# Optimization experiments

Hardware: AMD Instinct MI355X
Metric: run time of the kernel (lower is better)

Reference implementation:

```python
import jax, jax.numpy as jnp
import numpy as np

B, T = 16, 2048
D_MODEL, D_INNER, D_STATE, D_CONV, DT_RANK = 64, 128, 16, 4, 4

def leaky(x):
    return jnp.where(x >= 0, x, 0.01 * x)

def silu(x):
    return x * jax.nn.sigmoid(x)

def conv1d(x, w, b, pad):
    # x: (b,c,t), w: (o,i,k)
    y = jax.lax.conv_general_dilated(x, w, (1,), [(pad, pad)],
        dimension_numbers=('NCH', 'OIH', 'NCH'))
    return y + b[None, :, None]

def pixel_shuffle_1d(x, r):
    b, cr, t = x.shape
    c = cr // r
    return x.reshape(b, c, r, t).transpose(0, 1, 3, 2).reshape(b, c, t * r)

def rmsnorm(x, w, eps=1e-5):
    return x * jax.lax.rsqrt(jnp.mean(x * x, -1, keepdims=True) + eps) * w

def batchnorm(x, g, b, eps=1e-5):
    # training-mode BatchNorm1d: stats over (N, T) per channel
    mu = jnp.mean(x, axis=(0, 2), keepdims=True)
    var = jnp.var(x, axis=(0, 2), keepdims=True)
    return (x - mu) * jax.lax.rsqrt(var + eps) * g[None, :, None] + b[None, :, None]

def selective_scan(u, delta, A, Bm, Cm, D):
    # u, delta: (b,t,d); Bm, Cm: (b,t,n); A: (d,n); D: (d,)
    def step(h, inp):
        d_t, u_t, B_t, C_t = inp  # (b,d),(b,d),(b,n),(b,n)
        dA = jnp.exp(d_t[:, :, None] * A[None])              # (b,d,n)
        h = h * dA + (d_t * u_t)[:, :, None] * B_t[:, None, :]
        y = jnp.einsum('bdn,bn->bd', h, C_t)
        return h, y
    h0 = jnp.zeros((u.shape[0], A.shape[0], A.shape[1]), u.dtype)
    xs = tuple(jnp.swapaxes(a, 0, 1) for a in (delta, u, Bm, Cm))
    _, ys = jax.lax.scan(step, h0, xs)
    return jnp.swapaxes(ys, 0, 1) + u * D[None, None, :]

def mamba_layer(x, norm_w, in_proj_w, dwconv_w, dwconv_b, x_proj_w,
                dt_proj_w, dt_proj_b, A_log, D, out_proj_w):
    # x: (b,t,d_model); pre-norm residual Mamba block
    xn = rmsnorm(x, norm_w)
    xz = xn @ in_proj_w.T                                    # (b,t,2*d_inner)
    xm, z = jnp.split(xz, 2, axis=-1)
    # causal depthwise conv over time (pad left d_conv-1)
    xc = jax.lax.conv_general_dilated(jnp.swapaxes(xm, 1, 2), dwconv_w,
        (1,), [(D_CONV - 1, 0)], dimension_numbers=('NCH', 'OIH', 'NCH'),
        feature_group_count=D_INNER) + dwconv_b[None, :, None]
    xm = silu(jnp.swapaxes(xc, 1, 2))                        # (b,t,d_inner)
    x_dbl = xm @ x_proj_w.T                                  # (b,t,dt_rank+2n)
    dt, Bm, Cm = jnp.split(x_dbl, [DT_RANK, DT_RANK + D_STATE], axis=-1)
    delta = jax.nn.softplus(dt @ dt_proj_w.T + dt_proj_b)    # (b,t,d_inner)
    A = -jnp.exp(A_log)                                      # (d_inner,n)
    y = selective_scan(xm, delta, A, Bm, Cm, D)
    y = y * silu(z)
    return x + y @ out_proj_w.T

def setup_inputs():
    key = jax.random.key(0)
    ks = jax.random.split(key, 16)
    p = lambda k, shp, s=0.02: jax.random.normal(k, shp, jnp.float32) * s
    return {
        'x': jax.random.normal(ks[0], (B, 12, T), jnp.float32),
        'conv_in_w': p(ks[1], (D_MODEL, 12, 15)), 'conv_in_b': jnp.zeros((D_MODEL,), jnp.float32),
        'norm_w': jnp.ones((D_MODEL,), jnp.float32),
        'in_proj_w': p(ks[2], (2 * D_INNER, D_MODEL)),
        'dwconv_w': p(ks[3], (D_INNER, 1, D_CONV), 0.2), 'dwconv_b': jnp.zeros((D_INNER,), jnp.float32),
        'x_proj_w': p(ks[4], (DT_RANK + 2 * D_STATE, D_INNER)),
        'dt_proj_w': p(ks[5], (D_INNER, DT_RANK), 0.5),
        'dt_proj_b': jnp.full((D_INNER,), -2.0, jnp.float32),
        'A_log': jnp.tile(jnp.log(jnp.arange(1, D_STATE + 1, dtype=jnp.float32))[None], (D_INNER, 1)),
        'D': jnp.ones((D_INNER,), jnp.float32),
        'out_proj_w': p(ks[6], (D_MODEL, D_INNER)),
        'merge_w': p(ks[7], (D_MODEL, D_MODEL, 15)), 'merge_b': jnp.zeros((D_MODEL,), jnp.float32),
        'bn_g': jnp.ones((D_MODEL,), jnp.float32), 'bn_b': jnp.zeros((D_MODEL,), jnp.float32),
        'up1_w': p(ks[8], (320 * 5, D_MODEL, 15)), 'up1_b': jnp.zeros((320 * 5,), jnp.float32),
        'up2_w': p(ks[9], (128 * 2, 320, 15)), 'up2_b': jnp.zeros((128 * 2,), jnp.float32),
        'out_w': p(ks[10], (12, 128, 15)), 'out_b': jnp.zeros((12,), jnp.float32),
    }

def reference(x, conv_in_w, conv_in_b, norm_w, in_proj_w, dwconv_w, dwconv_b,
              x_proj_w, dt_proj_w, dt_proj_b, A_log, D, out_proj_w,
              merge_w, merge_b, bn_g, bn_b, up1_w, up1_b, up2_w, up2_b,
              out_w, out_b):
    h = leaky(conv1d(x, conv_in_w, conv_in_b, 7))            # (b,64,t)
    hold = h
    s = mamba_layer(jnp.swapaxes(h, 1, 2), norm_w, in_proj_w, dwconv_w,
                    dwconv_b, x_proj_w, dt_proj_w, dt_proj_b, A_log, D,
                    out_proj_w)
    h2 = jnp.swapaxes(s, 1, 2)                               # (b,64,t)
    m = batchnorm(conv1d(h2, merge_w, merge_b, 7), bn_g, bn_b) + hold
    u5 = leaky(pixel_shuffle_1d(conv1d(m, up1_w, up1_b, 7), 5))    # (b,320,5t)
    u10 = leaky(pixel_shuffle_1d(conv1d(u5, up2_w, up2_b, 7), 2))  # (b,128,10t)
    return conv1d(u10, out_w, out_b, 7)                      # (b,12,10t)
```

## Files before the change

kernel.cpp:

```cpp
#include <hip/hip_runtime.h>
#include <hip/hip_bf16.h>
#include <math.h>

typedef __hip_bfloat16 bf16;
typedef __attribute__((ext_vector_type(8))) short short8;
typedef __attribute__((ext_vector_type(4))) float f32x4;

#define BB 16
#define TT 2048
#define DM 64
#define DI 128
#define DSN 16
#define NCHK 32
#define CLEN 64

union U8 { int4 i4; unsigned short u[8]; };

__device__ __forceinline__ bf16  f2b(float v){ return __float2bfloat16(v); }
__device__ __forceinline__ float b2f(bf16 v){ return __bfloat162float(v); }
__device__ __forceinline__ unsigned short f2bu(float v){
  bf16 b = __float2bfloat16(v); unsigned short u; __builtin_memcpy(&u,&b,2); return u;
}
__device__ __forceinline__ float bu2f(unsigned short u){
  unsigned int x = ((unsigned int)u) << 16; float f; __builtin_memcpy(&f,&x,4); return f;
}
__device__ __forceinline__ float siluf(float x){ return x / (1.f + __expf(-x)); }
__device__ __forceinline__ float leakyf(float x){ return x >= 0.f ? x : 0.01f*x; }
__device__ __forceinline__ float softplusf(float x){ return x > 20.f ? x : log1pf(__expf(x)); }

struct PackCfg { const float* w; short* wp; int COUT, CIN, NTg, NCH, NTAP, fragOff; };
struct PackArgs { PackCfg c[7]; int totalFrags; float* stats; };

__global__ __launch_bounds__(256) void k_pack_all(PackArgs a)
{
  int i = blockIdx.x*256 + threadIdx.x;
  if (blockIdx.x == 0 && threadIdx.x < 128) a.stats[threadIdx.x] = 0.f;
  int lane = i & 63, frag = i >> 6;
  if (frag >= a.totalFrags) return;
  int ci_ = 0;
  #pragma unroll
  for (int q = 1; q < 7; q++) if (frag >= a.c[q].fragOff) ci_ = q;
  const PackCfg& C = a.c[ci_];
  int lf = frag - C.fragOff;
  int cot = lf % C.NTg; int kc = lf / C.NTg;
  int ch = kc % C.NCH;  int k  = kc / C.NCH;
  int co = cot*16 + (lane & 15);
  int ci0 = ch*32 + (lane >> 4)*8;
  unsigned short v[8];
  #pragma unroll
  for (int j = 0; j < 8; j++)
    v[j] = (co < C.COUT) ? f2bu(C.w[((size_t)co*C.CIN + ci0 + j)*C.NTAP + k]) : (unsigned short)0;
  short* dst = C.wp + (size_t)lf*512 + lane*8;
  *(int4*)dst = *(int4*)v;
}

__global__ __launch_bounds__(256) void k_conv_in(
    const float* __restrict__ x, const float* __restrict__ w,
    const float* __restrict__ bias, bf16* __restrict__ ht)
{
  __shared__ float sx[12][272];
  __shared__ float sw[12][15];
  int tid = threadIdx.x;
  int t0 = blockIdx.x * 256;
  int co = blockIdx.y;
  int b  = blockIdx.z;
  for (int i = tid; i < 12*15; i += 256) sw[i/15][i%15] = w[co*180 + i];
  for (int i = tid; i < 12*270; i += 256) {
    int ci = i/270, L = i%270;
    int tt = t0 - 7 + L;
    sx[ci][L] = (tt >= 0 && tt < TT) ? x[((size_t)b*12+ci)*TT + tt] : 0.f;
  }
  __syncthreads();
  float acc = bias[co];
  #pragma unroll
  for (int ci = 0; ci < 12; ci++) {
    #pragma unroll
    for (int k = 0; k < 15; k++)
      acc += sx[ci][tid+k]*sw[ci][k];
  }
  acc = leakyf(acc);
  int t = t0 + tid;
  ht[((size_t)b*TT + t)*DM + co] = f2b(acc);
}

__global__ __launch_bounds__(256) void k_inproj_mfma(
    const bf16* __restrict__ ht, const float* __restrict__ nw,
    const short* __restrict__ wp, bf16* __restrict__ xm, bf16* __restrict__ z)
{
  __shared__ short sxa[64*128];
  __shared__ float sred[64][4];
  const int tid = threadIdx.x;
  const int lane = tid & 63, wv = tid >> 6;
  const int lnm = lane & 15, quad = lane >> 4;
  const size_t bt0 = (size_t)blockIdx.x * 64;

  {
    int row = tid >> 2, part = tid & 3, ch0 = part*16;
    const short* src = (const short*)ht + (bt0 + row)*64 + ch0;
    U8 p0, p1; p0.i4 = *(const int4*)src; p1.i4 = *(const int4*)(src + 8);
    float f[16]; float ss = 0.f;
    #pragma unroll
    for (int j = 0; j < 8; j++) { f[j] = bu2f(p0.u[j]); f[8+j] = bu2f(p1.u[j]); }
    #pragma unroll
    for (int j = 0; j < 16; j++) ss += f[j]*f[j];
    sred[row][part] = ss;
    __syncthreads();
    float tot = sred[row][0]+sred[row][1]+sred[row][2]+sred[row][3];
    float sc = rsqrtf(tot*(1.f/64.f) + 1e-5f);
    U8 o0, o1;
    #pragma unroll
    for (int j = 0; j < 8; j++) {
      o0.u[j] = f2bu(f[j]  *sc*nw[ch0+j]);
      o1.u[j] = f2bu(f[8+j]*sc*nw[ch0+8+j]);
    }
    int s0 = part*2, s1 = part*2+1;
    *(int4*)(sxa + row*128 + ((s0 ^ (row&7))<<3)) = o0.i4;
    *(int4*)(sxa + row*128 + ((s1 ^ (row&7))<<3)) = o1.i4;
  }
  __syncthreads();

  f32x4 acc[4][4];
  #pragma unroll
  for (int m = 0; m < 4; m++)
    #pragma unroll
    for (int n = 0; n < 4; n++) acc[m][n] = (f32x4){0.f,0.f,0.f,0.f};

  #pragma unroll
  for (int kc = 0; kc < 2; kc++) {
    short8 bfr[4];
    #pragma unroll
    for (int n = 0; n < 4; n++) {
      int fid = kc*16 + wv*4 + n;
      bfr[n] = *(const short8*)(wp + (size_t)fid*512 + lane*8);
    }
    #pragma unroll
    for (int m = 0; m < 4; m++) {
      int r2 = m*16 + lnm;
      short8 a = *(const short8*)(sxa + r2*128 + (((kc*4+quad) ^ (r2&7))<<3));
      #pragma unroll
      for (int n = 0; n < 4; n++)
        acc[m][n] = __builtin_amdgcn_mfma_f32_16x16x32_bf16(a, bfr[n], acc[m][n], 0, 0, 0);
    }
  }

  #pragma unroll
  for (int m = 0; m < 4; m++)
    #pragma unroll
    for (int n = 0; n < 4; n++) {
      int co = wv*64 + n*16 + lnm;
      float v[4] = {acc[m][n].x, acc[m][n].y, acc[m][n].z, acc[m][n].w};
      #pragma unroll
      for (int r = 0; r < 4; r++) {
        size_t t = bt0 + m*16 + quad*4 + r;
        if (co < 128) xm[t*128 + co]       = f2b(v[r]);
        else          z [t*128 + (co-128)] = f2b(v[r]);
      }
    }
}

__global__ __launch_bounds__(256) void k_dwconv(
    const bf16* __restrict__ xm, const float* __restrict__ w,
    const float* __restrict__ bias, bf16* __restrict__ xcb)
{
  int idx = blockIdx.x*256 + threadIdx.x;
  int c = idx & (DI-1);
  int bt = idx >> 7;
  int t = bt & (TT-1);
  float acc = bias[c];
  #pragma unroll
  for (int k = 0; k < 4; k++) {
    int tt = t - 3 + k;
    if (tt >= 0) acc += b2f(xm[(size_t)(bt - 3 + k)*DI + c]) * w[c*4+k];
  }
  xcb[idx] = f2b(siluf(acc));
}

__global__ __launch_bounds__(256) void k_xproj_mfma(
    const bf16* __restrict__ xcb, const short* __restrict__ wp, float* __restrict__ xd)
{
  __shared__ __align__(16) char smem[256*64];
  const int tid = threadIdx.x;
  const int lane = tid & 63, wv = tid >> 6;
  const int lnm = lane & 15, quad = lane >> 4;
  const size_t bt0 = (size_t)blockIdx.x * 256;
  const int wvt = wv*64;

  f32x4 acc[4][3];
  #pragma unroll
  for (int m = 0; m < 4; m++)
    #pragma unroll
    for (int n = 0; n < 3; n++) acc[m][n] = (f32x4){0.f,0.f,0.f,0.f};

  for (int ch = 0; ch < 4; ch++) {
    __syncthreads();
    int sl = tid & 3;
    for (int r = tid >> 2; r < 256; r += 64) {
      int4 v = *(const int4*)((const short*)xcb + (bt0 + r)*128 + ch*32 + sl*8);
      *(int4*)(&smem[r*64 + ((sl ^ ((r>>1) & 3)) << 4)]) = v;
    }
    __syncthreads();
    short8 bfr[3];
    #pragma unroll
    for (int n = 0; n < 3; n++)
      bfr[n] = *(const short8*)(wp + (size_t)(ch*3+n)*512 + lane*8);
    #pragma unroll
    for (int m = 0; m < 4; m++) {
      int row = wvt + m*16 + lnm;
      short8 a = *(const short8*)(&smem[row*64 + ((quad ^ ((row>>1) & 3)) << 4)]);
      #pragma unroll
      for (int n = 0; n < 3; n++)
        acc[m][n] = __builtin_amdgcn_mfma_f32_16x16x32_bf16(a, bfr[n], acc[m][n], 0, 0, 0);
    }
  }
  #pragma unroll
  for (int m = 0; m < 4; m++)
    #pragma unroll
    for (int n = 0; n < 3; n++) {
      int cho = n*16 + lnm;
      float v[4] = {acc[m][n].x, acc[m][n].y, acc[m][n].z, acc[m][n].w};
      #pragma unroll
      for (int r = 0; r < 4; r++) {
        size_t t = bt0 + wvt + m*16 + quad*4 + r;
        xd[t*48 + cho] = v[r];
      }
    }
}

__global__ __launch_bounds__(256) void k_delta(
    const float* __restrict__ xd, const float* __restrict__ w,
    const float* __restrict__ bias, float* __restrict__ dlt)
{
  int idx = blockIdx.x*256 + threadIdx.x;
  int c = idx & (DI-1);
  int bt = idx >> 7;
  const float* dt = xd + (size_t)bt*48;
  float acc = bias[c];
  #pragma unroll
  for (int r = 0; r < 4; r++) acc += dt[r]*w[c*4+r];
  dlt[idx] = softplusf(acc);
}

__global__ __launch_bounds__(256) void k_scan_sum(
    const float* __restrict__ dlt, const bf16* __restrict__ xcb,
    const float* __restrict__ xd, const float* __restrict__ A_log,
    float* __restrict__ gP, float* __restrict__ gS)
{
  int tid = threadIdx.x;
  int n = tid & 15, dl = tid >> 4;
  int d = blockIdx.x*16 + dl;
  int b = blockIdx.y, ck = blockIdx.z;
  float A = -__expf(A_log[d*DSN + n]);
  float P = 1.f, h = 0.f;
  size_t base = (size_t)b*TT + (size_t)ck*CLEN;
  for (int i = 0; i < CLEN; i++) {
    size_t ib = base + i;
    float dd = dlt[ib*DI + d];
    float uu = b2f(xcb[ib*DI + d]);
    float Bv = xd [ib*48 + 4 + n];
    float dA = __expf(dd*A);
    h = h*dA + dd*uu*Bv;
    P *= dA;
  }
  size_t idx = (((size_t)b*NCHK + ck)*DI + d)*DSN + n;
  gP[idx] = P; gS[idx] = h;
}

__global__ __launch_bounds__(256) void k_scan_comb(
    const float* __restrict__ gP, const float* __restrict__ gS,
    float* __restrict__ ghs)
{
  int idx = blockIdx.x*256 + threadIdx.x;
  int n = idx & 15, d = (idx >> 4) & 127, b = idx >> 11;
  float h = 0.f;
  for (int c = 0; c < NCHK; c++) {
    size_t j = (((size_t)b*NCHK + c)*DI + d)*DSN + n;
    ghs[j] = h;
    h = gP[j]*h + gS[j];
  }
}

__global__ __launch_bounds__(256) void k_scan_out(
    const float* __restrict__ dlt, const bf16* __restrict__ xcb,
    const float* __restrict__ xd, const float* __restrict__ A_log,
    const float* __restrict__ Dv, const float* __restrict__ ghs,
    bf16* __restrict__ y)
{
  int tid = threadIdx.x;
  int n = tid & 15, dl = tid >> 4;
  int d = blockIdx.x*16 + dl;
  int b = blockIdx.y, ck = blockIdx.z;
  float A = -__expf(A_log[d*DSN + n]);
  float Dd = Dv[d];
  size_t idx = (((size_t)b*NCHK + ck)*DI + d)*DSN + n;
  float h = ghs[idx];
  size_t base = (size_t)b*TT + (size_t)ck*CLEN;
  for (int i = 0; i < CLEN; i++) {
    size_t ib = base + i;
    float dd = dlt[ib*DI + d];
    float uu = b2f(xcb[ib*DI + d]);
    float Bv = xd [ib*48 + 4  + n];
    float Cv = xd [ib*48 + 20 + n];
    float dA = __expf(dd*A);
    h = h*dA + dd*uu*Bv;
    float c = h*Cv;
    c += __shfl_xor(c, 1); c += __shfl_xor(c, 2);
    c += __shfl_xor(c, 4); c += __shfl_xor(c, 8);
    if (n == 0) y[ib*DI + d] = f2b(c + uu*Dd);
  }
}

__global__ __launch_bounds__(256) void k_outproj_mfma(
    const bf16* __restrict__ gy, const bf16* __restrict__ gz,
    const bf16* __restrict__ ht, const short* __restrict__ wp,
    bf16* __restrict__ st)
{
  __shared__ __align__(16) char smem[256*64];
  const int tid = threadIdx.x;
  const int lane = tid & 63, wv = tid >> 6;
  const int lnm = lane & 15, quad = lane >> 4;
  const size_t bt0 = (size_t)blockIdx.x * 256;
  const int wvt = wv*64;

  f32x4 acc[4][4];
  #pragma unroll
  for (int m = 0; m < 4; m++)
    #pragma unroll
    for (int n = 0; n < 4; n++) acc[m][n] = (f32x4){0.f,0.f,0.f,0.f};

  for (int ch = 0; ch < 4; ch++) {
    __syncthreads();
    int sl = tid & 3;
    for (int r = tid >> 2; r < 256; r += 64) {
      size_t base = (bt0 + r)*(size_t)DI + ch*32 + sl*8;
      U8 yy; yy.i4 = *(const int4*)((const short*)gy + base);
      U8 zz; zz.i4 = *(const int4*)((const short*)gz + base);
      U8 o;
      #pragma unroll
      for (int j = 0; j < 8; j++)
        o.u[j] = f2bu(bu2f(yy.u[j]) * siluf(bu2f(zz.u[j])));
      *(int4*)(&smem[r*64 + ((sl ^ ((r>>1) & 3)) << 4)]) = o.i4;
    }
    __syncthreads();
    short8 bfr[4];
    #pragma unroll
    for (int n = 0; n < 4; n++)
      bfr[n] = *(const short8*)(wp + (size_t)(ch*4+n)*512 + lane*8);
    #pragma unroll
    for (int m = 0; m < 4; m++) {
      int row = wvt + m*16 + lnm;
      short8 a = *(const short8*)(&smem[row*64 + ((quad ^ ((row>>1) & 3)) << 4)]);
      #pragma unroll
      for (int n = 0; n < 4; n++)
        acc[m][n] = __builtin_amdgcn_mfma_f32_16x16x32_bf16(a, bfr[n], acc[m][n], 0, 0, 0);
    }
  }
  #pragma unroll
  for (int m = 0; m < 4; m++)
    #pragma unroll
    for (int n = 0; n < 4; n++) {
      int cho = n*16 + lnm;
      float v[4] = {acc[m][n].x, acc[m][n].y, acc[m][n].z, acc[m][n].w};
      #pragma unroll
      for (int r = 0; r < 4; r++) {
        size_t t = bt0 + wvt + m*16 + quad*4 + r;
        st[t*DM + cho] = f2b(v[r] + b2f(ht[t*DM + cho]));
      }
    }
}

template<int CIN, int MSUB, int NSUB, int R, bool LEAKY, bool STATS, int OUTMODE>
__global__ __launch_bounds__(256) void mfma_conv(
    const bf16* __restrict__ inp, const short* __restrict__ wp,
    const float* __restrict__ bias, void* __restrict__ outv,
    float* __restrict__ stats, int Tlen, int NTg)
{
  constexpr int NCH = CIN/32;
  constexpr int NC  = 16*NSUB;
  constexpr int NCR = NC/R;
  constexpr int TBLK = 4*MSUB*16;
  constexpr int ROWS = TBLK + 14;
  constexpr int ROWW = 32;
  constexpr int STAGE_B = ROWS*ROWW*2;
  constexpr int EPI_B = (OUTMODE==0) ? 4*16*NC*2 : 4*16*68*4;
  constexpr int LDSB = (STAGE_B > EPI_B) ? STAGE_B : EPI_B;
  __shared__ __align__(16) char smem[LDSB];
  short* sx = (short*)smem;

  const int tid  = threadIdx.x;
  const int lane = tid & 63;
  const int wv   = tid >> 6;
  const int lnm  = lane & 15;
  const int quad = lane >> 4;
  const int t0   = blockIdx.x * TBLK;
  const int by   = blockIdx.y;
  const int b    = blockIdx.z;
  const int wvt  = wv*(MSUB*16);

  f32x4 acc[MSUB][NSUB];
  #pragma unroll
  for (int m = 0; m < MSUB; m++)
    #pragma unroll
    for (int n = 0; n < NSUB; n++)
      acc[m][n] = (f32x4){0.f,0.f,0.f,0.f};

  for (int ch = 0; ch < NCH; ch++) {
    __syncthreads();
    for (int i = tid; i < ROWS*4; i += 256) {
      int r = i >> 2, sl = i & 3;
      int t = t0 - 7 + r;
      int4 v = {0,0,0,0};
      if (t >= 0 && t < Tlen)
        v = *(const int4*)(inp + ((size_t)b*Tlen + t)*CIN + ch*32 + sl*8);
      *(int4*)(sx + r*ROWW + ((sl ^ ((r>>1) & 3)) << 3)) = v;
    }
    __syncthreads();

    short8 bcur[NSUB], bnxt[NSUB];
    #pragma unroll
    for (int n = 0; n < NSUB; n++) {
      size_t fid = (size_t)((0*NCH + ch)*NTg + by*NSUB + n);
      bcur[n] = *(const short8*)(wp + fid*512 + lane*8);
    }
    for (int k = 0; k < 15; k++) {
      if (k < 14) {
        #pragma unroll
        for (int n = 0; n < NSUB; n++) {
          size_t fid = (size_t)(((k+1)*NCH + ch)*NTg + by*NSUB + n);
          bnxt[n] = *(const short8*)(wp + fid*512 + lane*8);
        }
      }
      short8 af[MSUB];
      #pragma unroll
      for (int m = 0; m < MSUB; m++) {
        int row = wvt + m*16 + lnm + k;
        af[m] = *(const short8*)(sx + row*ROWW + ((quad ^ ((row>>1) & 3)) << 3));
      }
      #pragma unroll
      for (int m = 0; m < MSUB; m++)
        #pragma unroll
        for (int n = 0; n < NSUB; n++)
          acc[m][n] = __builtin_amdgcn_mfma_f32_16x16x32_bf16(af[m], bcur[n], acc[m][n], 0, 0, 0);
      #pragma unroll
      for (int n = 0; n < NSUB; n++) bcur[n] = bnxt[n];
    }
  }

  #pragma unroll
  for (int n = 0; n < NSUB; n++) {
    float bv = bias[by*NC + n*16 + lnm];
    #pragma unroll
    for (int m = 0; m < MSUB; m++) {
      acc[m][n].x += bv; acc[m][n].y += bv; acc[m][n].z += bv; acc[m][n].w += bv;
    }
  }
  if (STATS) {
    #pragma unroll
    for (int n = 0; n < NSUB; n++) {
      float s1 = 0.f, s2 = 0.f;
      #pragma unroll
      for (int m = 0; m < MSUB; m++) {
        f32x4 a = acc[m][n];
        s1 += a.x + a.y + a.z + a.w;
        s2 += a.x*a.x + a.y*a.y + a.z*a.z + a.w*a.w;
      }
      s1 += __shfl_xor(s1, 16); s1 += __shfl_xor(s1, 32);
      s2 += __shfl_xor(s2, 16); s2 += __shfl_xor(s2, 32);
      if (quad == 0) {
        atomicAdd(&stats[by*NC + n*16 + lnm], s1);
        atomicAdd(&stats[64 + by*NC + n*16 + lnm], s2);
      }
    }
  }
  if (LEAKY) {
    #pragma unroll
    for (int m = 0; m < MSUB; m++)
      #pragma unroll
      for (int n = 0; n < NSUB; n++) {
        acc[m][n].x = leakyf(acc[m][n].x); acc[m][n].y = leakyf(acc[m][n].y);
        acc[m][n].z = leakyf(acc[m][n].z); acc[m][n].w = leakyf(acc[m][n].w);
      }
  }

  __syncthreads();

  if (OUTMODE == 0) {
    const int CTOT = NTg*16/R;
    bf16* outp = (bf16*)outv;
    size_t brow = (size_t)b * ((size_t)Tlen*R);
    short* Cw = (short*)smem + wv*16*NC;
    #pragma unroll
    for (int m = 0; m < MSUB; m++) {
      #pragma unroll
      for (int n = 0; n < NSUB; n++) {
        int cof = n*16 + lnm;
        int p = cof % R, c = cof / R;
        float vv[4] = {acc[m][n].x, acc[m][n].y, acc[m][n].z, acc[m][n].w};
        #pragma unroll
        for (int r = 0; r < 4; r++) {
          int t = quad*4 + r;
          Cw[t*NC + p*NCR + c] = (short)f2bu(vv[r]);
        }
      }
      const int SPT = NC/8;
      for (int j = lane; j < 16*SPT; j += 64) {
        int t = j / SPT, sl = j % SPT;
        int cosw = sl*8;
        int p = cosw / NCR, coff = cosw % NCR;
        int tout = (t0 + wvt + m*16 + t)*R + p;
        size_t ga = (brow + tout)*(size_t)CTOT + (size_t)by*NCR + coff;
        *(int4*)((short*)outp + ga) = *(const int4*)(Cw + t*NC + cosw);
      }
    }
  } else {
    float* Cw = (float*)smem + wv*(16*68);
    #pragma unroll
    for (int m = 0; m < MSUB; m++) {
      float vv[4] = {acc[m][0].x, acc[m][0].y, acc[m][0].z, acc[m][0].w};
      #pragma unroll
      for (int r = 0; r < 4; r++) {
        int t = m*16 + quad*4 + r;
        Cw[lnm*68 + t] = vv[r];
      }
    }
    float* outf = (float*)outv;
    for (int j = lane; j < 12*16; j += 64) {
      int co = j >> 4, t4 = (j & 15)*4;
      size_t ga = ((size_t)b*12 + co)*(size_t)Tlen + t0 + wvt + t4;
      *(float4*)(outf + ga) = *(const float4*)(Cw + co*68 + t4);
    }
  }
}

__global__ __launch_bounds__(256) void k_bnadd2(
    const bf16* __restrict__ m2, const float* __restrict__ stats,
    const float* __restrict__ g, const float* __restrict__ bb,
    const bf16* __restrict__ ht, bf16* __restrict__ mt)
{
  int idx = blockIdx.x*256 + threadIdx.x;
  int c = idx & 63;
  const float cnt = (float)(BB*TT);
  float mu  = stats[c] / cnt;
  float var = stats[64+c] / cnt - mu*mu;
  float inv = rsqrtf(var + 1e-5f);
  float v = b2f(m2[idx]);
  mt[idx] = f2b((v - mu)*inv*g[c] + bb[c] + b2f(ht[idx]));
}

extern "C" void kernel_launch(void* const* d_in, const int* in_sizes, int n_in,
                              void* d_out, int out_size, void* d_ws, size_t ws_size,
                              hipStream_t stream)
{
  const float* in_x       = (const float*)d_in[0];
  const float* conv_in_w  = (const float*)d_in[1];
  const float* conv_in_b  = (const float*)d_in[2];
  const float* norm_w     = (const float*)d_in[3];
  const float* in_proj_w  = (const float*)d_in[4];
  const float* dwconv_w   = (const float*)d_in[5];
  const float* dwconv_b   = (const float*)d_in[6];
  const float* x_proj_w   = (const float*)d_in[7];
  const float* dt_proj_w  = (const float*)d_in[8];
  const float* dt_proj_b  = (const float*)d_in[9];
  const float* A_log      = (const float*)d_in[10];
  const float* Dvec       = (const float*)d_in[11];
  const float* out_proj_w = (const float*)d_in[12];
  const float* merge_w    = (const float*)d_in[13];
  const float* merge_b    = (const float*)d_in[14];
  const float* bn_g       = (const float*)d_in[15];
  const float* bn_b       = (const float*)d_in[16];
  const float* up1_w      = (const float*)d_in[17];
  const float* up1_b      = (const float*)d_in[18];
  const float* up2_w      = (const float*)d_in[19];
  const float* up2_b      = (const float*)d_in[20];
  const float* out_w      = (const float*)d_in[21];
  const float* out_b      = (const float*)d_in[22];
  float* out = (float*)d_out;

  size_t off = 0;
  auto take = [&](size_t bytes) -> void* {
    void* p = (char*)d_ws + off;
    off += (bytes + 255) & ~(size_t)255;
    return p;
  };
  const size_t F_BDMT = (size_t)BB*DM*TT;
  const size_t F_BTDI = (size_t)BB*TT*DI;
  bf16*  g_ht  = (bf16*) take(F_BDMT*2);
  bf16*  g_st  = (bf16*) take(F_BDMT*2);
  bf16*  g_m2  = (bf16*) take(F_BDMT*2);
  bf16*  g_mt  = (bf16*) take(F_BDMT*2);
  float* g_stt = (float*)take(512);
  short* wp_mg = (short*)take((size_t)15*2*4 *512*2);
  short* wp_u1 = (short*)take((size_t)15*2*100*512*2);
  short* wp_u2 = (short*)take((size_t)15*10*16*512*2);
  short* wp_oc = (short*)take((size_t)15*4*1  *512*2);
  short* wp_ip = (short*)take((size_t)1*2*16*512*2);
  short* wp_xp = (short*)take((size_t)1*4*3 *512*2);
  short* wp_op = (short*)take((size_t)1*4*4 *512*2);
  size_t mamba_base = off;
  bf16*  g_xm  = (bf16*) take(F_BTDI*2);
  bf16*  g_z   = (bf16*) take(F_BTDI*2);
  bf16*  g_xcb = (bf16*) take(F_BTDI*2);
  float* g_xd  = (float*)take((size_t)BB*TT*48*4);
  float* g_dl  = (float*)take(F_BTDI*4);
  bf16*  g_y   = (bf16*) take(F_BTDI*2);
  float* g_P   = (float*)take((size_t)BB*NCHK*DI*DSN*4);
  float* g_S   = (float*)take((size_t)BB*NCHK*DI*DSN*4);
  float* g_hs  = (float*)take((size_t)BB*NCHK*DI*DSN*4);
  const size_t U10_B = (size_t)BB*20480*128*2;
  if (off < mamba_base + U10_B) off = mamba_base + U10_B;
  bf16*  g_u10 = (bf16*)((char*)d_ws + mamba_base);
  bf16*  g_u5  = (bf16*)take((size_t)BB*10240*320*2);
  if (off > ws_size) return;

  {
    PackArgs pa;
    int o0 = 0;
    auto C = [&](int i, const float* w, short* wp, int COUT, int CIN, int NTg, int NCH, int NTAP){
      pa.c[i] = {w, wp, COUT, CIN, NTg, NCH, NTAP, o0};
      o0 += NTAP*NCH*NTg;
    };
    C(0, merge_w,    wp_mg, 64,   64,  4,   2,  15);
    C(1, up1_w,      wp_u1, 1600, 64,  100, 2,  15);
    C(2, up2_w,      wp_u2, 256,  320, 16,  10, 15);
    C(3, out_w,      wp_oc, 12,   128, 1,   4,  15);
    C(4, in_proj_w,  wp_ip, 256,  64,  16,  2,  1);
    C(5, x_proj_w,   wp_xp, 36,   128, 3,   4,  1);
    C(6, out_proj_w, wp_op, 64,   128, 4,   4,  1);
    pa.totalFrags = o0;
    pa.stats = g_stt;
    k_pack_all<<<(o0*64 + 255)/256, 256, 0, stream>>>(pa);
  }

  k_conv_in<<<dim3(TT/256, DM, BB), 256, 0, stream>>>(in_x, conv_in_w, conv_in_b, g_ht);

  k_inproj_mfma<<<BB*TT/64, 256, 0, stream>>>(g_ht, norm_w, wp_ip, g_xm, g_z);
  k_dwconv<<<BB*TT*DI/256, 256, 0, stream>>>(g_xm, dwconv_w, dwconv_b, g_xcb);
  k_xproj_mfma<<<BB*TT/256, 256, 0, stream>>>(g_xcb, wp_xp, g_xd);
  k_delta<<<BB*TT*DI/256, 256, 0, stream>>>(g_xd, dt_proj_w, dt_proj_b, g_dl);
  k_scan_sum<<<dim3(DI/16, BB, NCHK), 256, 0, stream>>>(g_dl, g_xcb, g_xd, A_log, g_P, g_S);
  k_scan_comb<<<BB*DI*DSN/256, 256, 0, stream>>>(g_P, g_S, g_hs);
  k_scan_out<<<dim3(DI/16, BB, NCHK), 256, 0, stream>>>(g_dl, g_xcb, g_xd, A_log, Dvec, g_hs, g_y);
  k_outproj_mfma<<<BB*TT/256, 256, 0, stream>>>(g_y, g_z, g_ht, wp_op, g_st);

  mfma_conv<64,4,4,1,false,true,0><<<dim3(TT/256, 1, BB), 256, 0, stream>>>(
      g_st, wp_mg, merge_b, g_m2, g_stt, TT, 4);
  k_bnadd2<<<BB*TT*64/256, 256, 0, stream>>>(g_m2, g_stt, bn_g, bn_b, g_ht, g_mt);

  mfma_conv<64,4,5,5,true,false,0><<<dim3(TT/256, 20, BB), 256, 0, stream>>>(
      g_mt, wp_u1, up1_b, g_u5, nullptr, TT, 100);

  mfma_conv<320,4,4,2,true,false,0><<<dim3(TT*5/256, 4, BB), 256, 0, stream>>>(
      g_u5, wp_u2, up2_b, g_u10, nullptr, TT*5, 16);

  mfma_conv<128,4,1,1,false,false,1><<<dim3(TT*10/256, 1, BB), 256, 0, stream>>>(
      g_u10, wp_oc, out_b, out, nullptr, TT*10, 1);
}
```

Before: 859.1 us.

## Fuse delta into scan kernels, shrink proj tiles, use direct global-to-LDS loads

The separate k_delta kernel and its fp32 delta buffer are removed. Both scan kernels now recompute softplus(dt_proj) inline from the x_proj output, which trades a full-size global write and two reads for extra per-step arithmetic. The x_proj and out_proj GEMMs move to 64-row blocks with one M-subtile per wave, giving four times as many blocks. The x_proj kernel and the conv staging now use global_load_lds to copy straight into LDS, which drops the XOR swizzle and so risks LDS bank conflicts on fragment reads.

After: 1.162 ms. +35.2%, slower.

```diff
diff --git a/kernel.cpp b/kernel.cpp
--- a/kernel.cpp
+++ b/kernel.cpp
@@ -27,6 +27,12 @@
 __device__ __forceinline__ float siluf(float x){ return x / (1.f + __expf(-x)); }
 __device__ __forceinline__ float leakyf(float x){ return x >= 0.f ? x : 0.01f*x; }
 __device__ __forceinline__ float softplusf(float x){ return x > 20.f ? x : log1pf(__expf(x)); }
+
+__device__ __forceinline__ void gload_lds16(const void* g, void* l){
+  __builtin_amdgcn_global_load_lds(
+      (const __attribute__((address_space(1))) void*)g,
+      (__attribute__((address_space(3))) void*)l, 16, 0, 0);
+}
 
 struct PackCfg { const float* w; short* wp; int COUT, CIN, NTg, NCH, NTAP, fragOff; };
 struct PackArgs { PackCfg c[7]; int totalFrags; float* stats; };
@@ -178,85 +184,66 @@
 __global__ __launch_bounds__(256) void k_xproj_mfma(
     const bf16* __restrict__ xcb, const short* __restrict__ wp, float* __restrict__ xd)
 {
-  __shared__ __align__(16) char smem[256*64];
+  __shared__ __align__(16) short sx[64*32];
   const int tid = threadIdx.x;
   const int lane = tid & 63, wv = tid >> 6;
   const int lnm = lane & 15, quad = lane >> 4;
-  const size_t bt0 = (size_t)blockIdx.x * 256;
-  const int wvt = wv*64;
-
-  f32x4 acc[4][3];
-  #pragma unroll
-  for (int m = 0; m < 4; m++)
-    #pragma unroll
-    for (int n = 0; n < 3; n++) acc[m][n] = (f32x4){0.f,0.f,0.f,0.f};
+  const size_t bt0 = (size_t)blockIdx.x * 64;
+
+  f32x4 acc[3];
+  #pragma unroll
+  for (int n = 0; n < 3; n++) acc[n] = (f32x4){0.f,0.f,0.f,0.f};
 
   for (int ch = 0; ch < 4; ch++) {
     __syncthreads();
-    int sl = tid & 3;
-    for (int r = tid >> 2; r < 256; r += 64) {
-      int4 v = *(const int4*)((const short*)xcb + (bt0 + r)*128 + ch*32 + sl*8);
-      *(int4*)(&smem[r*64 + ((sl ^ ((r>>1) & 3)) << 4)]) = v;
+    {
+      int r = tid >> 2, sl = tid & 3;
+      short* lp = sx + wv*512;
+      gload_lds16((const short*)xcb + (bt0 + r)*128 + ch*32 + sl*8, lp);
     }
     __syncthreads();
     short8 bfr[3];
     #pragma unroll
     for (int n = 0; n < 3; n++)
       bfr[n] = *(const short8*)(wp + (size_t)(ch*3+n)*512 + lane*8);
-    #pragma unroll
-    for (int m = 0; m < 4; m++) {
-      int row = wvt + m*16 + lnm;
-      short8 a = *(const short8*)(&smem[row*64 + ((quad ^ ((row>>1) & 3)) << 4)]);
-      #pragma unroll
-      for (int n = 0; n < 3; n++)
-        acc[m][n] = __builtin_amdgcn_mfma_f32_16x16x32_bf16(a, bfr[n], acc[m][n], 0, 0, 0);
-    }
-  }
-  #pragma unroll
-  for (int m = 0; m < 4; m++)
-    #pragma unroll
-    for (int n = 0; n < 3; n++) {
-      int cho = n*16 + lnm;
-      float v[4] = {acc[m][n].x, acc[m][n].y, acc[m][n].z, acc[m][n].w};
-      #pragma unroll
-      for (int r = 0; r < 4; r++) {
-        size_t t = bt0 + wvt + m*16 + quad*4 + r;
-        xd[t*48 + cho] = v[r];
-      }
-    }
-}
-
-__global__ __launch_bounds__(256) void k_delta(
-    const float* __restrict__ xd, const float* __restrict__ w,
-    const float* __restrict__ bias, float* __restrict__ dlt)
-{
-  int idx = blockIdx.x*256 + threadIdx.x;
-  int c = idx & (DI-1);
-  int bt = idx >> 7;
-  const float* dt = xd + (size_t)bt*48;
-  float acc = bias[c];
-  #pragma unroll
-  for (int r = 0; r < 4; r++) acc += dt[r]*w[c*4+r];
-  dlt[idx] = softplusf(acc);
+    int row = wv*16 + lnm;
+    short8 a = *(const short8*)(sx + row*32 + quad*8);
+    #pragma unroll
+    for (int n = 0; n < 3; n++)
+      acc[n] = __builtin_amdgcn_mfma_f32_16x16x32_bf16(a, bfr[n], acc[n], 0, 0, 0);
+  }
+  #pragma unroll
+  for (int n = 0; n < 3; n++) {
+    int cho = n*16 + lnm;
+    float v[4] = {acc[n].x, acc[n].y, acc[n].z, acc[n].w};
+    #pragma unroll
+    for (int r = 0; r < 4; r++) {
+      size_t t = bt0 + wv*16 + quad*4 + r;
+      xd[t*48 + cho] = v[r];
+    }
+  }
 }
 
 __global__ __launch_bounds__(256) void k_scan_sum(
-    const float* __restrict__ dlt, const bf16* __restrict__ xcb,
-    const float* __restrict__ xd, const float* __restrict__ A_log,
-    float* __restrict__ gP, float* __restrict__ gS)
+    const bf16* __restrict__ xcb, const float* __restrict__ xd,
+    const float* __restrict__ A_log, const float* __restrict__ dtw,
+    const float* __restrict__ dtb, float* __restrict__ gP, float* __restrict__ gS)
 {
   int tid = threadIdx.x;
   int n = tid & 15, dl = tid >> 4;
   int d = blockIdx.x*16 + dl;
   int b = blockIdx.y, ck = blockIdx.z;
   float A = -__expf(A_log[d*DSN + n]);
+  float w0 = dtw[d*4], w1 = dtw[d*4+1], w2 = dtw[d*4+2], w3 = dtw[d*4+3];
+  float bd = dtb[d];
   float P = 1.f, h = 0.f;
   size_t base = (size_t)b*TT + (size_t)ck*CLEN;
   for (int i = 0; i < CLEN; i++) {
     size_t ib = base + i;
-    float dd = dlt[ib*DI + d];
+    const float* xr = xd + ib*48;
+    float dd = softplusf(bd + xr[0]*w0 + xr[1]*w1 + xr[2]*w2 + xr[3]*w3);
     float uu = b2f(xcb[ib*DI + d]);
-    float Bv = xd [ib*48 + 4 + n];
+    float Bv = xr[4 + n];
     float dA = __expf(dd*A);
     h = h*dA + dd*uu*Bv;
     P *= dA;
@@ -280,26 +267,29 @@
 }
 
 __global__ __launch_bounds__(256) void k_scan_out(
-    const float* __restrict__ dlt, const bf16* __restrict__ xcb,
-    const float* __restrict__ xd, const float* __restrict__ A_log,
-    const float* __restrict__ Dv, const float* __restrict__ ghs,
-    bf16* __restrict__ y)
+    const bf16* __restrict__ xcb, const float* __restrict__ xd,
+    const float* __restrict__ A_log, const float* __restrict__ dtw,
+    const float* __restrict__ dtb, const float* __restrict__ Dv,
+    const float* __restrict__ ghs, bf16* __restrict__ y)
 {
   int tid = threadIdx.x;
   int n = tid & 15, dl = tid >> 4;
   int d = blockIdx.x*16 + dl;
   int b = blockIdx.y, ck = blockIdx.z;
   float A = -__expf(A_log[d*DSN + n]);
+  float w0 = dtw[d*4], w1 = dtw[d*4+1], w2 = dtw[d*4+2], w3 = dtw[d*4+3];
+  float bd = dtb[d];
   float Dd = Dv[d];
   size_t idx = (((size_t)b*NCHK + ck)*DI + d)*DSN + n;
   float h = ghs[idx];
   size_t base = (size_t)b*TT + (size_t)ck*CLEN;
   for (int i = 0; i < CLEN; i++) {
     size_t ib = base + i;
-    float dd = dlt[ib*DI + d];
+    const float* xr = xd + ib*48;
+    float dd = softplusf(bd + xr[0]*w0 + xr[1]*w1 + xr[2]*w2 + xr[3]*w3);
     float uu = b2f(xcb[ib*DI + d]);
-    float Bv = xd [ib*48 + 4  + n];
-    float Cv = xd [ib*48 + 20 + n];
+    float Bv = xr[4  + n];
+    float Cv = xr[20 + n];
     float dA = __expf(dd*A);
     h = h*dA + dd*uu*Bv;
     float c = h*Cv;
@@ -314,23 +304,20 @@
     const bf16* __restrict__ ht, const short* __restrict__ wp,
     bf16* __restrict__ st)
 {
-  __shared__ __align__(16) char smem[256*64];
+  __shared__ __align__(16) short sx[64*32];
   const int tid = threadIdx.x;
   const int lane = tid & 63, wv = tid >> 6;
   const int lnm = lane & 15, quad = lane >> 4;
-  const size_t bt0 = (size_t)blockIdx.x * 256;
-  const int wvt = wv*64;
-
-  f32x4 acc[4][4];
-  #pragma unroll
-  for (int m = 0; m < 4; m++)
-    #pragma unroll
-    for (int n = 0; n < 4; n++) acc[m][n] = (f32x4){0.f,0.f,0.f,0.f};
+  const size_t bt0 = (size_t)blockIdx.x * 64;
+
+  f32x4 acc[4];
+  #pragma unroll
+  for (int n = 0; n < 4; n++) acc[n] = (f32x4){0.f,0.f,0.f,0.f};
 
   for (int ch = 0; ch < 4; ch++) {
     __syncthreads();
-    int sl = tid & 3;
-    for (int r = tid >> 2; r < 256; r += 64) {
+    {
+      int r = tid >> 2, sl = tid & 3;
       size_t base = (bt0 + r)*(size_t)DI + ch*32 + sl*8;
       U8 yy; yy.i4 = *(const int4*)((const short*)gy + base);
       U8 zz; zz.i4 = *(const int4*)((const short*)gz + base);
@@ -338,34 +325,29 @@
       #pragma unroll
       for (int j = 0; j < 8; j++)
         o.u[j] = f2bu(bu2f(yy.u[j]) * siluf(bu2f(zz.u[j])));
-      *(int4*)(&smem[r*64 + ((sl ^ ((r>>1) & 3)) << 4)]) = o.i4;
+      *(int4*)(sx + tid*8) = o.i4;
     }
     __syncthreads();
     short8 bfr[4];
     #pragma unroll
     for (int n = 0; n < 4; n++)
       bfr[n] = *(const short8*)(wp + (size_t)(ch*4+n)*512 + lane*8);
-    #pragma unroll
-    for (int m = 0; m < 4; m++) {
-      int row = wvt + m*16 + lnm;
-      short8 a = *(const short8*)(&smem[row*64 + ((quad ^ ((row>>1) & 3)) << 4)]);
-      #pragma unroll
-      for (int n = 0; n < 4; n++)
-        acc[m][n] = __builtin_amdgcn_mfma_f32_16x16x32_bf16(a, bfr[n], acc[m][n], 0, 0, 0);
-    }
-  }
-  #pragma unroll
-  for (int m = 0; m < 4; m++)
-    #pragma unroll
-    for (int n = 0; n < 4; n++) {
-      int cho = n*16 + lnm;
-      float v[4] = {acc[m][n].x, acc[m][n].y, acc[m][n].z, acc[m][n].w};
-      #pragma unroll
-      for (int r = 0; r < 4; r++) {
-        size_t t = bt0 + wvt + m*16 + quad*4 + r;
-        st[t*DM + cho] = f2b(v[r] + b2f(ht[t*DM + cho]));
-      }
-    }
+    int row = wv*16 + lnm;
+    short8 a = *(const short8*)(sx + row*32 + quad*8);
+    #pragma unroll
+    for (int n = 0; n < 4; n++)
+      acc[n] = __builtin_amdgcn_mfma_f32_16x16x32_bf16(a, bfr[n], acc[n], 0, 0, 0);
+  }
+  #pragma unroll
+  for (int n = 0; n < 4; n++) {
+    int cho = n*16 + lnm;
+    float v[4] = {acc[n].x, acc[n].y, acc[n].z, acc[n].w};
+    #pragma unroll
+    for (int r = 0; r < 4; r++) {
+      size_t t = bt0 + wv*16 + quad*4 + r;
+      st[t*DM + cho] = f2b(v[r] + b2f(ht[t*DM + cho]));
+    }
+  }
 }
 
 template<int CIN, int MSUB, int NSUB, int R, bool LEAKY, bool STATS, int OUTMODE>
@@ -380,6 +362,7 @@
   constexpr int TBLK = 4*MSUB*16;
   constexpr int ROWS = TBLK + 14;
   constexpr int ROWW = 32;
+  constexpr int NSLOT = ROWS*4;
   constexpr int STAGE_B = ROWS*ROWW*2;
   constexpr int EPI_B = (OUTMODE==0) ? 4*16*NC*2 : 4*16*68*4;
   constexpr int LDSB = (STAGE_B > EPI_B) ? STAGE_B : EPI_B;
@@ -405,13 +388,19 @@
 
   for (int ch = 0; ch < NCH; ch++) {
     __syncthreads();
-    for (int i = tid; i < ROWS*4; i += 256) {
-      int r = i >> 2, sl = i & 3;
-      int t = t0 - 7 + r;
-      int4 v = {0,0,0,0};
-      if (t >= 0 && t < Tlen)
-        v = *(const int4*)(inp + ((size_t)b*Tlen + t)*CIN + ch*32 + sl*8);
-      *(int4*)(sx + r*ROWW + ((sl ^ ((r>>1) & 3)) << 3)) = v;
+    #pragma unroll
+    for (int j = 0; j*256 < NSLOT; j++) {
+      int i = j*256 + tid;
+      if (i < NSLOT) {
+        int r = i >> 2, sl = i & 3;
+        int t = t0 - 7 + r;
+        if (t >= 0 && t < Tlen) {
+          short* lp = sx + (j*256 + wv*64)*8;
+          gload_lds16(inp + ((size_t)b*Tlen + t)*CIN + ch*32 + sl*8, lp);
+        } else {
+          *(int4*)(sx + (size_t)i*8) = (int4){0,0,0,0};
+        }
+      }
     }
     __syncthreads();
 
@@ -433,7 +422,7 @@
       #pragma unroll
       for (int m = 0; m < MSUB; m++) {
         int row = wvt + m*16 + lnm + k;
-        af[m] = *(const short8*)(sx + row*ROWW + ((quad ^ ((row>>1) & 3)) << 3));
+        af[m] = *(const short8*)(sx + row*ROWW + quad*8);
       }
       #pragma unroll
       for (int m = 0; m < MSUB; m++)
@@ -600,7 +589,6 @@
   bf16*  g_z   = (bf16*) take(F_BTDI*2);
   bf16*  g_xcb = (bf16*) take(F_BTDI*2);
   float* g_xd  = (float*)take((size_t)BB*TT*48*4);
-  float* g_dl  = (float*)take(F_BTDI*4);
   bf16*  g_y   = (bf16*) take(F_BTDI*2);
   float* g_P   = (float*)take((size_t)BB*NCHK*DI*DSN*4);
   float* g_S   = (float*)take((size_t)BB*NCHK*DI*DSN*4);
@@ -634,12 +622,11 @@
 
   k_inproj_mfma<<<BB*TT/64, 256, 0, stream>>>(g_ht, norm_w, wp_ip, g_xm, g_z);
   k_dwconv<<<BB*TT*DI/256, 256, 0, stream>>>(g_xm, dwconv_w, dwconv_b, g_xcb);
-  k_xproj_mfma<<<BB*TT/256, 256, 0, stream>>>(g_xcb, wp_xp, g_xd);
-  k_delta<<<BB*TT*DI/256, 256, 0, stream>>>(g_xd, dt_proj_w, dt_proj_b, g_dl);
-  k_scan_sum<<<dim3(DI/16, BB, NCHK), 256, 0, stream>>>(g_dl, g_xcb, g_xd, A_log, g_P, g_S);
+  k_xproj_mfma<<<BB*TT/64, 256, 0, stream>>>(g_xcb, wp_xp, g_xd);
+  k_scan_sum<<<dim3(DI/16, BB, NCHK), 256, 0, stream>>>(g_xcb, g_xd, A_log, dt_proj_w, dt_proj_b, g_P, g_S);
   k_scan_comb<<<BB*DI*DSN/256, 256, 0, stream>>>(g_P, g_S, g_hs);
-  k_scan_out<<<dim3(DI/16, BB, NCHK), 256, 0, stream>>>(g_dl, g_xcb, g_xd, A_log, Dvec, g_hs, g_y);
-  k_outproj_mfma<<<BB*TT/256, 256, 0, stream>>>(g_y, g_z, g_ht, wp_op, g_st);
+  k_scan_out<<<dim3(DI/16, BB, NCHK), 256, 0, stream>>>(g_xcb, g_xd, A_log, dt_proj_w, dt_proj_b, Dvec, g_hs, g_y);
+  k_outproj_mfma<<<BB*TT/64, 256, 0, stream>>>(g_y, g_z, g_ht, wp_op, g_st);
 
   mfma_conv<64,4,4,1,false,true,0><<<dim3(TT/256, 1, BB), 256, 0, stream>>>(
       g_st, wp_mg, merge_b, g_m2, g_stt, TT, 4);
```
